# Optimization experiments

Hardware: AMD Instinct MI355X
Metric: run time of the kernel (lower is better)

Reference implementation:

```python
import jax, jax.numpy as jnp
import numpy as np

EPS = 1e-5
TEMP = 50.0


def setup_inputs() -> dict:
    key = jax.random.key(0)
    features = jax.random.normal(key, (4, 64, 128, 128), dtype=jnp.float32)
    return {"features": features, "patch_sim_neiref_neisimavgsize": 5}


def reference(features, patch_sim_neiref_neisimavgsize):
    k = patch_sim_neiref_neisimavgsize
    B, C, H, W = features.shape
    pad = k // 2
    xp = jnp.pad(features, ((0, 0), (0, 0), (pad, pad), (pad, pad)))
    # windows ordered (kh, kw) to match F.unfold: [B, k*k, C, H, W]
    wins = jnp.stack([xp[:, :, i:i + H, j:j + W]
                      for i in range(k) for j in range(k)], axis=1)
    # [B, H, W, k*k, C]
    patch = jnp.transpose(wins, (0, 3, 4, 1, 2)) + EPS
    patch_norm = patch / jnp.sqrt(jnp.sum(patch * patch, axis=-1, keepdims=True))
    center = patch_norm[..., (k * k) // 2:(k * k) // 2 + 1, :]  # center pixel of window
    sim = jnp.sum(patch_norm * center, axis=-1, keepdims=True)   # cosine sim [B,H,W,kk,1]
    wei = jax.nn.softmax(TEMP * sim, axis=-2)
    repr_vec = jnp.sum(patch * wei, axis=-2)                     # [B,H,W,C]
    return jnp.transpose(repr_vec, (0, 3, 1, 2))                 # [B,C,H,W]
```

## Files before the change

### kernel.cpp

```cpp
#include <hip/hip_runtime.h>

#define EPS 1e-5f
#define TEMP 50.0f
#define CCH 64
#define HH 128
#define WW 128
#define HWSZ (HH * WW)
#define CEPS2 (CCH * EPS * EPS)

#define IT 8
#define HT 12
#define HPX (HT * HT)
#define HPAD 145

typedef _Float16 h16;
typedef h16 h2v __attribute__((ext_vector_type(2)));
typedef h16 h8v __attribute__((ext_vector_type(8)));
union H8 { h8v v; h2v p[4]; };

__device__ __forceinline__ float fdot2(h2v a, h2v b, float c) {
#if __has_builtin(__builtin_amdgcn_fdot2)
    return __builtin_amdgcn_fdot2(a, b, c, false);
#else
    return c + (float)a[0] * (float)b[0] + (float)a[1] * (float)b[1];
#endif
}

#define TP_PAD 72
__global__ __launch_bounds__(256) void rv_transpose(const float* __restrict__ x,
                                                    h16* __restrict__ xt) {
    __shared__ h16 buf[WW][TP_PAD];
    const int t = threadIdx.x;
    const int h = blockIdx.x;
    const int b = blockIdx.y;
    const float* src = x + (size_t)b * (CCH * HWSZ) + h * WW;
#pragma unroll 8
    for (int i = 0; i < 32; ++i) {
        int k = i * 256 + t;
        int c = k >> 7;
        int w = k & 127;
        buf[w][c] = (h16)src[(size_t)c * HWSZ + w];
    }
    __syncthreads();
    h16* dst = xt + (size_t)(b * HH + h) * WW * CCH;
#pragma unroll
    for (int j = 0; j < 4; ++j) {
        int idx = j * 256 + t;
        int w = idx >> 3;
        int q = idx & 7;
        h8v v = *(const h8v*)&buf[w][q * 8];
        *(h8v*)&dst[(size_t)w * CCH + q * 8] = v;
    }
}

__global__ __launch_bounds__(128) void rv_fused(const h16* __restrict__ xt,
                                                float* __restrict__ out) {
    __shared__ h8v  tile[8][HPAD];
    __shared__ float sh_q[HPX];

    const int t  = threadIdx.x;
    const int w0 = blockIdx.x * IT;
    const int h0 = blockIdx.y * IT;
    const int b  = blockIdx.z;

#pragma unroll
    for (int it = 0; it < 9; ++it) {
        int k = it * 128 + t;
        int q  = k & 7;
        int px = k >> 3;
        int row = px / HT;
        int col = px - row * HT;
        int gh = h0 + row - 2;
        int gw = w0 + col - 2;
        h8v v = {};
        if (gh >= 0 && gh < HH && gw >= 0 && gw < WW) {
            v = *(const h8v*)&xt[((size_t)(b * HH + gh) * WW + gw) * CCH + q * 8];
        }
        tile[q][px] = v;
    }
    __syncthreads();

    for (int idx = t; idx < HPX; idx += 128) {
        float q = 0.f;
#pragma unroll
        for (int hq = 0; hq < 8; ++hq) {
            H8 u; u.v = tile[hq][idx];
#pragma unroll
            for (int j = 0; j < 4; ++j) q = fdot2(u.p[j], u.p[j], q);
        }
        sh_q[idx] = q;
    }

    const int half = t & 1;
    const int pix  = t >> 1;
    const int r    = pix >> 3;
    const int c    = pix & 7;
    const int cpx  = (r + 2) * HT + (c + 2);

    H8 ctr[4];
#pragma unroll
    for (int g = 0; g < 4; ++g) ctr[g].v = tile[4 * half + g][cpx];

    float D[25];
#pragma unroll
    for (int dr = 0; dr < 5; ++dr) {
#pragma unroll
        for (int dc = 0; dc < 5; ++dc) {
            const int npx = (r + dr) * HT + (c + dc);
            float d = 0.f;
#pragma unroll
            for (int g = 0; g < 4; ++g) {
                H8 a; a.v = tile[4 * half + g][npx];
#pragma unroll
                for (int j = 0; j < 4; ++j) d = fdot2(ctr[g].p[j], a.p[j], d);
            }
            D[dr * 5 + dc] = d;
        }
    }
#pragma unroll
    for (int n = 0; n < 25; ++n) D[n] += __shfl_xor(D[n], 1);

    __syncthreads();

    const float N2c = sh_q[cpx] + CEPS2;
    float lg[25];
    float m = -1e30f;
#pragma unroll
    for (int dr = 0; dr < 5; ++dr) {
#pragma unroll
        for (int dc = 0; dc < 5; ++dc) {
            const int n = dr * 5 + dc;
            const int npx = (r + dr) * HT + (c + dc);
            const float N2n = sh_q[npx] + CEPS2;
            const float sim = (D[n] + CEPS2) * rsqrtf(N2n * N2c);
            lg[n] = TEMP * sim;
            m = fmaxf(m, lg[n]);
        }
    }
    float wei[25];
    float sum = 0.f;
#pragma unroll
    for (int n = 0; n < 25; ++n) {
        wei[n] = __expf(lg[n] - m);
        sum += wei[n];
    }
    const float rs = 1.f / sum;
#pragma unroll
    for (int n = 0; n < 25; ++n) wei[n] *= rs;

    h2v acc2[16];
#pragma unroll
    for (int i = 0; i < 16; ++i) acc2[i] = (h2v){(h16)0.f, (h16)0.f};
#pragma unroll
    for (int dr = 0; dr < 5; ++dr) {
#pragma unroll
        for (int dc = 0; dc < 5; ++dc) {
            const int npx = (r + dr) * HT + (c + dc);
            const h16 wh = (h16)wei[dr * 5 + dc];
            const h2v w2 = {wh, wh};
#pragma unroll
            for (int g = 0; g < 4; ++g) {
                H8 a; a.v = tile[4 * half + g][npx];
#pragma unroll
                for (int j = 0; j < 4; ++j)
                    acc2[g * 4 + j] = a.p[j] * w2 + acc2[g * 4 + j];
            }
        }
    }

    const size_t obase = (size_t)b * (CCH * HWSZ)
                       + (size_t)(32 * half) * HWSZ
                       + (h0 + r) * WW + (w0 + c);
#pragma unroll
    for (int i = 0; i < 16; ++i) {
        out[obase + (size_t)(2 * i) * HWSZ]     = (float)acc2[i][0] + EPS;
        out[obase + (size_t)(2 * i + 1) * HWSZ] = (float)acc2[i][1] + EPS;
    }
}

extern "C" void kernel_launch(void* const* d_in, const int* in_sizes, int n_in,
                              void* d_out, int out_size, void* d_ws, size_t ws_size,
                              hipStream_t stream) {
    const float* x = (const float*)d_in[0];
    float* outp = (float*)d_out;
    h16* xt = (h16*)d_ws;

    rv_transpose<<<dim3(HH, 4), dim3(256), 0, stream>>>(x, xt);
    rv_fused<<<dim3(WW / IT, HH / IT, 4), dim3(128, 1, 1), 0, stream>>>(xt, outp);
}
```

Before: 83.79 us.

## Split channels four ways per pixel and fuse single-pass softmax accumulation

The fused kernel now uses 256 threads, with four threads per output pixel each owning 16 channels instead of two threads owning 32. Partial dot products are reduced with two shuffles. Since cosine similarity is at most 1, the softmax subtracts the fixed bound TEMP instead of a computed max, so weights are exponentiated and accumulated in one pass and normalised at the end. This drops the 25-element D/lg/wei arrays and the second pass over the tile, cutting register pressure to raise occupancy, at the cost of more shuffles and unnormalised fp16 accumulation.

```diff
diff --git a/kernel.cpp b/kernel.cpp
--- a/kernel.cpp
+++ b/kernel.cpp
@@ -53,7 +53,7 @@
     }
 }
 
-__global__ __launch_bounds__(128) void rv_fused(const h16* __restrict__ xt,
+__global__ __launch_bounds__(256) void rv_fused(const h16* __restrict__ xt,
                                                 float* __restrict__ out) {
     __shared__ h8v  tile[8][HPAD];
     __shared__ float sh_q[HPX];
@@ -64,117 +64,93 @@
     const int b  = blockIdx.z;
 
 #pragma unroll
-    for (int it = 0; it < 9; ++it) {
-        int k = it * 128 + t;
-        int q  = k & 7;
-        int px = k >> 3;
-        int row = px / HT;
-        int col = px - row * HT;
-        int gh = h0 + row - 2;
-        int gw = w0 + col - 2;
-        h8v v = {};
-        if (gh >= 0 && gh < HH && gw >= 0 && gw < WW) {
-            v = *(const h8v*)&xt[((size_t)(b * HH + gh) * WW + gw) * CCH + q * 8];
+    for (int it = 0; it < 5; ++it) {
+        int k = it * 256 + t;
+        if (k < 8 * HPX) {
+            int q  = k & 7;
+            int px = k >> 3;
+            int row = px / HT;
+            int col = px - row * HT;
+            int gh = h0 + row - 2;
+            int gw = w0 + col - 2;
+            h8v v = {};
+            if (gh >= 0 && gh < HH && gw >= 0 && gw < WW) {
+                v = *(const h8v*)&xt[((size_t)(b * HH + gh) * WW + gw) * CCH + q * 8];
+            }
+            tile[q][px] = v;
         }
-        tile[q][px] = v;
     }
     __syncthreads();
 
-    for (int idx = t; idx < HPX; idx += 128) {
+    if (t < HPX) {
         float q = 0.f;
 #pragma unroll
         for (int hq = 0; hq < 8; ++hq) {
-            H8 u; u.v = tile[hq][idx];
+            H8 u; u.v = tile[hq][t];
 #pragma unroll
             for (int j = 0; j < 4; ++j) q = fdot2(u.p[j], u.p[j], q);
         }
-        sh_q[idx] = q;
+        sh_q[t] = q;
     }
+    __syncthreads();
 
-    const int half = t & 1;
-    const int pix  = t >> 1;
-    const int r    = pix >> 3;
-    const int c    = pix & 7;
-    const int cpx  = (r + 2) * HT + (c + 2);
+    const int qg  = t & 3;
+    const int pix = t >> 2;
+    const int r   = pix >> 3;
+    const int cl  = pix & 7;
+    const int cpx = (r + 2) * HT + (cl + 2);
 
-    H8 ctr[4];
-#pragma unroll
-    for (int g = 0; g < 4; ++g) ctr[g].v = tile[4 * half + g][cpx];
+    const float rinvC = rsqrtf(sh_q[cpx] + CEPS2);
 
-    float D[25];
+    H8 ctr0, ctr1;
+    ctr0.v = tile[2 * qg][cpx];
+    ctr1.v = tile[2 * qg + 1][cpx];
+
+    h2v acc[8] = {};
+    float wsum = 0.f;
+
 #pragma unroll
     for (int dr = 0; dr < 5; ++dr) {
 #pragma unroll
         for (int dc = 0; dc < 5; ++dc) {
-            const int npx = (r + dr) * HT + (c + dc);
+            const int npx = (r + dr) * HT + (cl + dc);
+            H8 a0, a1;
+            a0.v = tile[2 * qg][npx];
+            a1.v = tile[2 * qg + 1][npx];
             float d = 0.f;
 #pragma unroll
-            for (int g = 0; g < 4; ++g) {
-                H8 a; a.v = tile[4 * half + g][npx];
+            for (int j = 0; j < 4; ++j) d = fdot2(ctr0.p[j], a0.p[j], d);
 #pragma unroll
-                for (int j = 0; j < 4; ++j) d = fdot2(ctr[g].p[j], a.p[j], d);
-            }
-            D[dr * 5 + dc] = d;
-        }
-    }
-#pragma unroll
-    for (int n = 0; n < 25; ++n) D[n] += __shfl_xor(D[n], 1);
-
-    __syncthreads();
-
-    const float N2c = sh_q[cpx] + CEPS2;
-    float lg[25];
-    float m = -1e30f;
-#pragma unroll
-    for (int dr = 0; dr < 5; ++dr) {
-#pragma unroll
-        for (int dc = 0; dc < 5; ++dc) {
-            const int n = dr * 5 + dc;
-            const int npx = (r + dr) * HT + (c + dc);
+            for (int j = 0; j < 4; ++j) d = fdot2(ctr1.p[j], a1.p[j], d);
+            d += __shfl_xor(d, 1);
+            d += __shfl_xor(d, 2);
             const float N2n = sh_q[npx] + CEPS2;
-            const float sim = (D[n] + CEPS2) * rsqrtf(N2n * N2c);
-            lg[n] = TEMP * sim;
-            m = fmaxf(m, lg[n]);
-        }
-    }
-    float wei[25];
-    float sum = 0.f;
-#pragma unroll
-    for (int n = 0; n < 25; ++n) {
-        wei[n] = __expf(lg[n] - m);
-        sum += wei[n];
-    }
-    const float rs = 1.f / sum;
-#pragma unroll
-    for (int n = 0; n < 25; ++n) wei[n] *= rs;
-
-    h2v acc2[16];
-#pragma unroll
-    for (int i = 0; i < 16; ++i) acc2[i] = (h2v){(h16)0.f, (h16)0.f};
-#pragma unroll
-    for (int dr = 0; dr < 5; ++dr) {
-#pragma unroll
-        for (int dc = 0; dc < 5; ++dc) {
-            const int npx = (r + dr) * HT + (c + dc);
-            const h16 wh = (h16)wei[dr * 5 + dc];
+            const float sim = (d + CEPS2) * (rsqrtf(N2n) * rinvC);
+            const float wn = __expf(fmaf(TEMP, sim, -TEMP));
+            wsum += wn;
+            const h16 wh = (h16)wn;
             const h2v w2 = {wh, wh};
 #pragma unroll
-            for (int g = 0; g < 4; ++g) {
-                H8 a; a.v = tile[4 * half + g][npx];
-#pragma unroll
-                for (int j = 0; j < 4; ++j)
-                    acc2[g * 4 + j] = a.p[j] * w2 + acc2[g * 4 + j];
+            for (int j = 0; j < 4; ++j) {
+                acc[j]     = a0.p[j] * w2 + acc[j];
+                acc[4 + j] = a1.p[j] * w2 + acc[4 + j];
             }
         }
     }
 
+    const float rs = 1.f / wsum;
     const size_t obase = (size_t)b * (CCH * HWSZ)
-                       + (size_t)(32 * half) * HWSZ
-                       + (h0 + r) * WW + (w0 + c);
+                       + (size_t)(qg * 16) * HWSZ
+                       + (h0 + r) * WW + (w0 + cl);
 #pragma unroll
-    for (int i = 0; i < 16; ++i) {
-        out[obase + (size_t)(2 * i) * HWSZ]     = (float)acc2[i][0] + EPS;
-        out[obase + (size_t)(2 * i + 1) * HWSZ] = (float)acc2[i][1] + EPS;
+    for (int g = 0; g < 2; ++g) {
+#pragma unroll
+        for (int j = 0; j < 4; ++j) {
+            const float f0 = (float)acc[g * 4 + j][0];
+            const float f1 = (float)acc[g * 4 + j][1];
+            out[obase + (size_t)(g * 8 + 2 * j) * HWSZ]     = fmaf(f0, rs, EPS);
+            out[obase + (size_t)(g * 8 + 2 * j + 1) * HWSZ] = fmaf(f1, rs, EPS);
+        }
     }
 }
 
@@ -186,5 +162,5 @@
     h16* xt = (h16*)d_ws;
 
     rv_transpose<<<dim3(HH, 4), dim3(256), 0, stream>>>(x, xt);
-    rv_fused<<<dim3(WW / IT, HH / IT, 4), dim3(128, 1, 1), 0, stream>>>(xt, outp);
+    rv_fused<<<dim3(WW / IT, HH / IT, 4), dim3(256, 1, 1), 0, stream>>>(xt, outp);
 }
```

Result: no change. 82.45 us (-1.6%).
